# Kernel optimization log

Hardware: AMD Instinct MI355X
Metric: run time of the kernel (lower is better)

## Reference

```python
import jax, jax.numpy as jnp
import numpy as np

C, NHEAD, WIN = 192, 6, 8

def setup_inputs() -> dict:
    key = jax.random.key(0)
    ks = jax.random.split(key, 16)
    B, H, W = 4, 256, 256
    s = 0.02
    inp = {
        "q2d": jax.random.normal(ks[0], (B, C, H, W), jnp.float32),
        "kv2d": jax.random.normal(ks[1], (B, C, H, W), jnp.float32),
        "wq": jax.random.normal(ks[2], (C, C), jnp.float32) * s,
        "bq": jnp.zeros((C,), jnp.float32),
        "wk": jax.random.normal(ks[3], (C, C), jnp.float32) * s,
        "bk": jnp.zeros((C,), jnp.float32),
        "wv": jax.random.normal(ks[4], (C, C), jnp.float32) * s,
        "bv": jnp.zeros((C,), jnp.float32),
        "in_w": jax.random.normal(ks[5], (3 * C, C), jnp.float32) * s,
        "in_b": jnp.zeros((3 * C,), jnp.float32),
        "out_w": jax.random.normal(ks[6], (C, C), jnp.float32) * s,
        "out_b": jnp.zeros((C,), jnp.float32),
        "proj_w": jax.random.normal(ks[7], (C, C), jnp.float32) * s,
        "proj_b": jnp.zeros((C,), jnp.float32),
    }
    return inp

def _conv1x1(x, w, b):
    # x: [B,C,H,W], w: [O,C] (1x1 conv kernel), b: [O]
    return jnp.einsum('bchw,oc->bohw', x, w) + b[None, :, None, None]

def reference(q2d, kv2d, wq, bq, wk, bk, wv, bv, in_w, in_b, out_w, out_b, proj_w, proj_b):
    B, c, H, W = q2d.shape
    w = WIN
    Hb, Wb = H // w, W // w  # H,W chosen divisible by window -> pad is a no-op
    L = Hb * Wb
    S = w * w
    hd = c // NHEAD

    q = _conv1x1(q2d, wq, bq)
    k = _conv1x1(kv2d, wk, bk)
    v = _conv1x1(kv2d, wv, bv)

    def to_seq(t):
        # unfold(kernel=w, stride=w) -> blocks row-major over (Hb, Wb), tokens row-major within window
        return t.reshape(B, c, Hb, w, Wb, w).transpose(0, 2, 4, 3, 5, 1).reshape(B * L, S, c)

    qs, ks_, vs = to_seq(q), to_seq(k), to_seq(v)

    # nn.MultiheadAttention internal projections
    wq_i, wk_i, wv_i = jnp.split(in_w, 3, axis=0)
    bq_i, bk_i, bv_i = jnp.split(in_b, 3, axis=0)

    def heads(t, wgt, b):
        return (t @ wgt.T + b).reshape(B * L, S, NHEAD, hd).transpose(0, 2, 1, 3)

    qh = heads(qs, wq_i, bq_i)
    kh = heads(ks_, wk_i, bk_i)
    vh = heads(vs, wv_i, bv_i)

    scores = jnp.einsum('nhsd,nhtd->nhst', qh, kh) / jnp.sqrt(jnp.float32(hd))
    attn = jax.nn.softmax(scores, axis=-1)
    o = jnp.einsum('nhst,nhtd->nhsd', attn, vh)
    o = o.transpose(0, 2, 1, 3).reshape(B * L, S, c) @ out_w.T + out_b

    # fold back: [B*L, S, C] -> [B, C, H, W]
    o2d = o.reshape(B, Hb, Wb, w, w, c).transpose(0, 5, 1, 3, 2, 4).reshape(B, c, H, W)
    out = _conv1x1(o2d, proj_w, proj_b)
    return out + q2d
```

## Files before the change

kernel.cpp:

```cpp
#include <hip/hip_runtime.h>

#define CC 192
#define WFRAG_USHORTS (4*6*12*512)
#define SX 202
#define SV 74

typedef __attribute__((ext_vector_type(8))) short bf16x8;
typedef __attribute__((ext_vector_type(4))) float f32x4;

__device__ __forceinline__ unsigned short f2b(float f){
  unsigned u = __float_as_uint(f);
  return (unsigned short)((u + 0x7fffu + ((u >> 16) & 1u)) >> 16);
}
__device__ __forceinline__ unsigned pk2(float a, float b){
  return (unsigned)f2b(a) | ((unsigned)f2b(b) << 16);
}

__global__ void fuse_weights(const float* __restrict__ wq, const float* __restrict__ bq,
                             const float* __restrict__ wk, const float* __restrict__ bk,
                             const float* __restrict__ wv, const float* __restrict__ bv,
                             const float* __restrict__ in_w, const float* __restrict__ in_b,
                             const float* __restrict__ out_w, const float* __restrict__ out_b,
                             const float* __restrict__ proj_w, const float* __restrict__ proj_b,
                             unsigned short* __restrict__ Wf, float* __restrict__ Bf)
{
  int mat = blockIdx.x / CC, o = blockIdx.x % CC, ci = threadIdx.x;
  const float *A, *Bm, *bs, *ba; int aoff, boff; float scale = 1.f;
  if (mat == 0){ A=in_w; aoff=0;    Bm=wq;    bs=bq;    ba=in_b;   boff=0;    scale=0.17677669529663687f; }
  else if (mat==1){ A=in_w; aoff=CC;   Bm=wk;    bs=bk;    ba=in_b;   boff=CC;   }
  else if (mat==2){ A=in_w; aoff=2*CC; Bm=wv;    bs=bv;    ba=in_b;   boff=2*CC; }
  else            { A=proj_w; aoff=0;  Bm=out_w; bs=out_b; ba=proj_b; boff=0;    }
  const float* ar = A + (size_t)(aoff + o) * CC;
  float acc = 0.f;
  for (int m = 0; m < CC; ++m) acc = fmaf(ar[m], Bm[m*CC + ci], acc);
  int k = ci >> 5, n = o >> 4, lgv = (ci >> 3) & 3, e = ci & 7;
  int lane = (o & 15) | (lgv << 4);
  Wf[(((mat*6 + k)*12 + n) << 9) + lane*8 + e] = f2b(acc * scale);
  if (ci == 0){
    float bacc = 0.f;
    for (int m = 0; m < CC; ++m) bacc = fmaf(ar[m], bs[m], bacc);
    Bf[mat*CC + o] = (bacc + ba[boff + o]) * scale;
  }
}

__global__ __launch_bounds__(512, 4) void win_attn(
    const float* __restrict__ q2d, const float* __restrict__ kv2d,
    const unsigned short* __restrict__ Wf, const float* __restrict__ Bf,
    float* __restrict__ out)
{
  __shared__ unsigned short QK[2][64*SX];
  __shared__ unsigned short VT[192*SV];

  const int t = threadIdx.x;
  const int w = t >> 6, lane = t & 63, lr = lane & 15, lg = lane >> 4;
  const int bid = blockIdx.x;
  const int wid = (bid & 7) * 512 + (bid >> 3);
  const int b = wid >> 10, l = wid & 1023;
  const int y0 = (l >> 5) << 3, x0 = (l & 31) << 3;
  const float* qsrc  = q2d  + (size_t)b * CC * 65536;
  const float* kvsrc = kv2d + (size_t)b * CC * 65536;

  const int mat = w >> 2;
  const int tb  = 3 * (w & 3);

  auto stage = [&](const float* __restrict__ src, unsigned short* __restrict__ dst){
    #pragma unroll
    for (int i = 0; i < 3; ++i){
      int lin = i*512 + t;
      int c2 = lin >> 4, tok0 = (lin & 15) << 2;
      int gy = (y0 + (tok0 >> 3)) * 256 + x0 + (tok0 & 7);
      float4 va = *(const float4*)&src[(size_t)(2*c2)   * 65536 + gy];
      float4 vb = *(const float4*)&src[(size_t)(2*c2+1) * 65536 + gy];
      float fa[4] = {va.x, va.y, va.z, va.w};
      float fb[4] = {vb.x, vb.y, vb.z, vb.w};
      #pragma unroll
      for (int j = 0; j < 4; ++j)
        *(unsigned*)&dst[(tok0 + j)*SX + 2*c2] = pk2(fa[j], fb[j]);
    }
  };

  stage(qsrc,  QK[0]);
  stage(kvsrc, QK[1]);
  __syncthreads();

  const unsigned short* Xs = QK[mat];
  f32x4 qk[3][4] = {};
  f32x4 vv[3][2] = {};
  #pragma unroll
  for (int k = 0; k < 6; ++k){
    bf16x8 a[4];
    #pragma unroll
    for (int m = 0; m < 4; ++m)
      a[m] = *(const bf16x8*)&Xs[(m*16 + lr)*SX + k*32 + lg*8];
    bf16x8 av[2];
    #pragma unroll
    for (int mi = 0; mi < 2; ++mi)
      av[mi] = *(const bf16x8*)&QK[1][((2*mat + mi)*16 + lr)*SX + k*32 + lg*8];
    #pragma unroll
    for (int i = 0; i < 3; ++i){
      bf16x8 bw = *(const bf16x8*)&Wf[(((mat*6 + k)*12 + tb + i) << 9) + lane*8];
      #pragma unroll
      for (int m = 0; m < 4; ++m)
        qk[i][m] = __builtin_amdgcn_mfma_f32_16x16x32_bf16(a[m], bw, qk[i][m], 0, 0, 0);
      bf16x8 bv = *(const bf16x8*)&Wf[(((12 + k)*12 + tb + i) << 9) + lane*8];
      #pragma unroll
      for (int mi = 0; mi < 2; ++mi)
        vv[i][mi] = __builtin_amdgcn_mfma_f32_16x16x32_bf16(av[mi], bv, vv[i][mi], 0, 0, 0);
    }
  }
  #pragma unroll
  for (int i = 0; i < 3; ++i){
    int ch = (tb + i)*16 + lr;
    float bb = Bf[2*CC + ch];
    #pragma unroll
    for (int mi = 0; mi < 2; ++mi){
      int tk = (2*mat + mi)*16 + lg*4;
      *(unsigned*)&VT[ch*SV + tk]     = pk2(vv[i][mi][0] + bb, vv[i][mi][1] + bb);
      *(unsigned*)&VT[ch*SV + tk + 2] = pk2(vv[i][mi][2] + bb, vv[i][mi][3] + bb);
    }
  }
  __syncthreads();

  {
    unsigned short* dst = QK[mat];
    #pragma unroll
    for (int i = 0; i < 3; ++i){
      int ch = (tb + i)*16 + lr;
      float bb = Bf[mat*CC + ch];
      #pragma unroll
      for (int m = 0; m < 4; ++m)
        #pragma unroll
        for (int rr = 0; rr < 4; ++rr)
          dst[(m*16 + lg*4 + rr)*SX + ch] = f2b(qk[i][m][rr] + bb);
    }
  }
  __syncthreads();

  #pragma unroll
  for (int i = 0; i < 3; ++i){
    int task = 3*w + i;
    int h = task >> 2, r0 = (task & 3) << 4;
    f32x4 st[4] = {};
    bf16x8 bq_ = *(const bf16x8*)&QK[0][(r0 + lr)*SX + h*32 + lg*8];
    #pragma unroll
    for (int m = 0; m < 4; ++m){
      bf16x8 a = *(const bf16x8*)&QK[1][(m*16 + lr)*SX + h*32 + lg*8];
      st[m] = __builtin_amdgcn_mfma_f32_16x16x32_bf16(a, bq_, st[m], 0, 0, 0);
    }
    float mx = st[0][0];
    #pragma unroll
    for (int m = 0; m < 4; ++m)
      #pragma unroll
      for (int rr = 0; rr < 4; ++rr) mx = fmaxf(mx, st[m][rr]);
    mx = fmaxf(mx, __shfl_xor(mx, 16));
    mx = fmaxf(mx, __shfl_xor(mx, 32));
    float p[16]; float s = 0.f;
    #pragma unroll
    for (int m = 0; m < 4; ++m)
      #pragma unroll
      for (int rr = 0; rr < 4; ++rr){ float e = __expf(st[m][rr] - mx); p[m*4+rr] = e; s += e; }
    s += __shfl_xor(s, 16); s += __shfl_xor(s, 32);
    float inv = 1.f / s;
    #pragma unroll
    for (int i2 = 0; i2 < 16; ++i2) p[i2] *= inv;
    f32x4 o0 = {}, o1 = {};
    #pragma unroll
    for (int kt = 0; kt < 2; ++kt){
      bf16x8 ap;
      ((unsigned*)&ap)[0] = pk2(p[8*kt+0], p[8*kt+1]);
      ((unsigned*)&ap)[1] = pk2(p[8*kt+2], p[8*kt+3]);
      ((unsigned*)&ap)[2] = pk2(p[8*kt+4], p[8*kt+5]);
      ((unsigned*)&ap)[3] = pk2(p[8*kt+6], p[8*kt+7]);
      bf16x8 v0, v1;
      ((uint2*)&v0)[0] = *(const uint2*)&VT[(h*32 + lr)*SV      + kt*32 + lg*4];
      ((uint2*)&v0)[1] = *(const uint2*)&VT[(h*32 + lr)*SV      + kt*32 + 16 + lg*4];
      ((uint2*)&v1)[0] = *(const uint2*)&VT[(h*32 + 16 + lr)*SV + kt*32 + lg*4];
      ((uint2*)&v1)[1] = *(const uint2*)&VT[(h*32 + 16 + lr)*SV + kt*32 + 16 + lg*4];
      o0 = __builtin_amdgcn_mfma_f32_16x16x32_bf16(ap, v0, o0, 0, 0, 0);
      o1 = __builtin_amdgcn_mfma_f32_16x16x32_bf16(ap, v1, o1, 0, 0, 0);
    }
    #pragma unroll
    for (int rr = 0; rr < 4; ++rr){
      int tok = r0 + lg*4 + rr;
      QK[0][tok*SX + h*32 + lr]      = f2b(o0[rr]);
      QK[0][tok*SX + h*32 + 16 + lr] = f2b(o1[rr]);
    }
  }
  __syncthreads();

  {
    f32x4 eo[3][2] = {};
    #pragma unroll
    for (int k = 0; k < 6; ++k){
      bf16x8 bo[2];
      #pragma unroll
      for (int nt = 0; nt < 2; ++nt)
        bo[nt] = *(const bf16x8*)&QK[0][((2*mat + nt)*16 + lr)*SX + k*32 + lg*8];
      #pragma unroll
      for (int i = 0; i < 3; ++i){
        bf16x8 aw = *(const bf16x8*)&Wf[(((18 + k)*12 + tb + i) << 9) + lane*8];
        #pragma unroll
        for (int nt = 0; nt < 2; ++nt)
          eo[i][nt] = __builtin_amdgcn_mfma_f32_16x16x32_bf16(aw, bo[nt], eo[i][nt], 0, 0, 0);
      }
    }
    #pragma unroll
    for (int i = 0; i < 3; ++i){
      #pragma unroll
      for (int rr = 0; rr < 4; ++rr){
        int o = (tb + i)*16 + lg*4 + rr;
        float bb = Bf[3*CC + o];
        #pragma unroll
        for (int nt = 0; nt < 2; ++nt){
          int tok = (2*mat + nt)*16 + lr;
          size_t g = (size_t)(b*CC + o)*65536 + (size_t)(y0 + (tok >> 3))*256 + x0 + (tok & 7);
          out[g] = eo[i][nt][rr] + bb + q2d[g];
        }
      }
    }
  }
}

extern "C" void kernel_launch(void* const* d_in, const int* in_sizes, int n_in,
                              void* d_out, int out_size, void* d_ws, size_t ws_size,
                              hipStream_t stream)
{
  const float* q2d    = (const float*)d_in[0];
  const float* kv2d   = (const float*)d_in[1];
  const float* wq     = (const float*)d_in[2];
  const float* bq     = (const float*)d_in[3];
  const float* wk     = (const float*)d_in[4];
  const float* bk     = (const float*)d_in[5];
  const float* wv     = (const float*)d_in[6];
  const float* bv     = (const float*)d_in[7];
  const float* in_w   = (const float*)d_in[8];
  const float* in_b   = (const float*)d_in[9];
  const float* out_w  = (const float*)d_in[10];
  const float* out_b  = (const float*)d_in[11];
  const float* proj_w = (const float*)d_in[12];
  const float* proj_b = (const float*)d_in[13];

  unsigned short* Wf = (unsigned short*)d_ws;
  float* Bf = (float*)((char*)d_ws + WFRAG_USHORTS*2);
  float* out = (float*)d_out;

  fuse_weights<<<4*CC, CC, 0, stream>>>(wq,bq,wk,bk,wv,bv,in_w,in_b,
                                        out_w,out_b,proj_w,proj_b, Wf, Bf);
  win_attn<<<4096, 512, 0, stream>>>(q2d, kv2d, Wf, Bf, out);
}
```

Measured before the change: 347.0 us.

## Use six waves per window, keep V in registers, drop VT shared buffer

Shrinks the block from 8 to 6 waves so each wave owns one head's 32 channels, and computes V, Q and K projections in sequence over all 64 tokens. Each wave keeps its V tile in registers as MFMA B operands instead of writing a transposed VT array to LDS, and Q/K are written back in place with extra barriers. Removing VT cuts LDS per block, which is meant to let more blocks fit per CU (launch bounds 384,5). In exchange, register pressure per wave rises and each wave carries more serial MFMA work.

```diff
diff --git a/kernel.cpp b/kernel.cpp
--- a/kernel.cpp
+++ b/kernel.cpp
@@ -3,7 +3,6 @@
 #define CC 192
 #define WFRAG_USHORTS (4*6*12*512)
 #define SX 202
-#define SV 74
 
 typedef __attribute__((ext_vector_type(8))) short bf16x8;
 typedef __attribute__((ext_vector_type(4))) float f32x4;
@@ -43,13 +42,12 @@
   }
 }
 
-__global__ __launch_bounds__(512, 4) void win_attn(
+__global__ __launch_bounds__(384, 5) void win_attn(
     const float* __restrict__ q2d, const float* __restrict__ kv2d,
     const unsigned short* __restrict__ Wf, const float* __restrict__ Bf,
     float* __restrict__ out)
 {
   __shared__ unsigned short QK[2][64*SX];
-  __shared__ unsigned short VT[192*SV];
 
   const int t = threadIdx.x;
   const int w = t >> 6, lane = t & 63, lr = lane & 15, lg = lane >> 4;
@@ -59,14 +57,12 @@
   const int y0 = (l >> 5) << 3, x0 = (l & 31) << 3;
   const float* qsrc  = q2d  + (size_t)b * CC * 65536;
   const float* kvsrc = kv2d + (size_t)b * CC * 65536;
-
-  const int mat = w >> 2;
-  const int tb  = 3 * (w & 3);
+  const int tb2 = 2 * w;
 
   auto stage = [&](const float* __restrict__ src, unsigned short* __restrict__ dst){
     #pragma unroll
-    for (int i = 0; i < 3; ++i){
-      int lin = i*512 + t;
+    for (int i = 0; i < 4; ++i){
+      int lin = i*384 + t;
       int c2 = lin >> 4, tok0 = (lin & 15) << 2;
       int gy = (y0 + (tok0 >> 3)) * 256 + x0 + (tok0 & 7);
       float4 va = *(const float4*)&src[(size_t)(2*c2)   * 65536 + gy];
@@ -83,136 +79,169 @@
   stage(kvsrc, QK[1]);
   __syncthreads();
 
-  const unsigned short* Xs = QK[mat];
-  f32x4 qk[3][4] = {};
-  f32x4 vv[3][2] = {};
+  bf16x8 vp[2][2];
+  {
+    f32x4 vacc[2][4] = {};
+    #pragma unroll
+    for (int k = 0; k < 6; ++k){
+      bf16x8 a[4];
+      #pragma unroll
+      for (int m = 0; m < 4; ++m)
+        a[m] = *(const bf16x8*)&QK[1][(m*16 + lr)*SX + k*32 + lg*8];
+      #pragma unroll
+      for (int i = 0; i < 2; ++i){
+        bf16x8 bw = *(const bf16x8*)&Wf[(((12 + k)*12 + tb2 + i) << 9) + lane*8];
+        #pragma unroll
+        for (int m = 0; m < 4; ++m)
+          vacc[i][m] = __builtin_amdgcn_mfma_f32_16x16x32_bf16(a[m], bw, vacc[i][m], 0, 0, 0);
+      }
+    }
+    #pragma unroll
+    for (int i = 0; i < 2; ++i){
+      float bb = Bf[2*CC + (tb2 + i)*16 + lr];
+      #pragma unroll
+      for (int kt = 0; kt < 2; ++kt){
+        bf16x8 v;
+        ((unsigned*)&v)[0] = pk2(vacc[i][2*kt][0] + bb,   vacc[i][2*kt][1] + bb);
+        ((unsigned*)&v)[1] = pk2(vacc[i][2*kt][2] + bb,   vacc[i][2*kt][3] + bb);
+        ((unsigned*)&v)[2] = pk2(vacc[i][2*kt+1][0] + bb, vacc[i][2*kt+1][1] + bb);
+        ((unsigned*)&v)[3] = pk2(vacc[i][2*kt+1][2] + bb, vacc[i][2*kt+1][3] + bb);
+        vp[i][kt] = v;
+      }
+    }
+  }
+
+  f32x4 qacc[2][4] = {};
   #pragma unroll
   for (int k = 0; k < 6; ++k){
     bf16x8 a[4];
     #pragma unroll
     for (int m = 0; m < 4; ++m)
-      a[m] = *(const bf16x8*)&Xs[(m*16 + lr)*SX + k*32 + lg*8];
-    bf16x8 av[2];
-    #pragma unroll
-    for (int mi = 0; mi < 2; ++mi)
-      av[mi] = *(const bf16x8*)&QK[1][((2*mat + mi)*16 + lr)*SX + k*32 + lg*8];
-    #pragma unroll
-    for (int i = 0; i < 3; ++i){
-      bf16x8 bw = *(const bf16x8*)&Wf[(((mat*6 + k)*12 + tb + i) << 9) + lane*8];
-      #pragma unroll
-      for (int m = 0; m < 4; ++m)
-        qk[i][m] = __builtin_amdgcn_mfma_f32_16x16x32_bf16(a[m], bw, qk[i][m], 0, 0, 0);
-      bf16x8 bv = *(const bf16x8*)&Wf[(((12 + k)*12 + tb + i) << 9) + lane*8];
-      #pragma unroll
-      for (int mi = 0; mi < 2; ++mi)
-        vv[i][mi] = __builtin_amdgcn_mfma_f32_16x16x32_bf16(av[mi], bv, vv[i][mi], 0, 0, 0);
-    }
-  }
-  #pragma unroll
-  for (int i = 0; i < 3; ++i){
-    int ch = (tb + i)*16 + lr;
-    float bb = Bf[2*CC + ch];
-    #pragma unroll
-    for (int mi = 0; mi < 2; ++mi){
-      int tk = (2*mat + mi)*16 + lg*4;
-      *(unsigned*)&VT[ch*SV + tk]     = pk2(vv[i][mi][0] + bb, vv[i][mi][1] + bb);
-      *(unsigned*)&VT[ch*SV + tk + 2] = pk2(vv[i][mi][2] + bb, vv[i][mi][3] + bb);
-    }
+      a[m] = *(const bf16x8*)&QK[0][(m*16 + lr)*SX + k*32 + lg*8];
+    #pragma unroll
+    for (int i = 0; i < 2; ++i){
+      bf16x8 bw = *(const bf16x8*)&Wf[(((0*6 + k)*12 + tb2 + i) << 9) + lane*8];
+      #pragma unroll
+      for (int m = 0; m < 4; ++m)
+        qacc[i][m] = __builtin_amdgcn_mfma_f32_16x16x32_bf16(a[m], bw, qacc[i][m], 0, 0, 0);
+    }
+  }
+  __syncthreads();
+  #pragma unroll
+  for (int i = 0; i < 2; ++i){
+    int ch = (tb2 + i)*16 + lr;
+    float bb = Bf[0*CC + ch];
+    #pragma unroll
+    for (int m = 0; m < 4; ++m)
+      #pragma unroll
+      for (int rr = 0; rr < 4; ++rr)
+        QK[0][(m*16 + lg*4 + rr)*SX + ch] = f2b(qacc[i][m][rr] + bb);
+  }
+
+  f32x4 kacc[2][4] = {};
+  #pragma unroll
+  for (int k = 0; k < 6; ++k){
+    bf16x8 a[4];
+    #pragma unroll
+    for (int m = 0; m < 4; ++m)
+      a[m] = *(const bf16x8*)&QK[1][(m*16 + lr)*SX + k*32 + lg*8];
+    #pragma unroll
+    for (int i = 0; i < 2; ++i){
+      bf16x8 bw = *(const bf16x8*)&Wf[(((1*6 + k)*12 + tb2 + i) << 9) + lane*8];
+      #pragma unroll
+      for (int m = 0; m < 4; ++m)
+        kacc[i][m] = __builtin_amdgcn_mfma_f32_16x16x32_bf16(a[m], bw, kacc[i][m], 0, 0, 0);
+    }
+  }
+  __syncthreads();
+  #pragma unroll
+  for (int i = 0; i < 2; ++i){
+    int ch = (tb2 + i)*16 + lr;
+    float bb = Bf[1*CC + ch];
+    #pragma unroll
+    for (int m = 0; m < 4; ++m)
+      #pragma unroll
+      for (int rr = 0; rr < 4; ++rr)
+        QK[1][(m*16 + lg*4 + rr)*SX + ch] = f2b(kacc[i][m][rr] + bb);
   }
   __syncthreads();
 
   {
-    unsigned short* dst = QK[mat];
-    #pragma unroll
-    for (int i = 0; i < 3; ++i){
-      int ch = (tb + i)*16 + lr;
-      float bb = Bf[mat*CC + ch];
-      #pragma unroll
-      for (int m = 0; m < 4; ++m)
-        #pragma unroll
-        for (int rr = 0; rr < 4; ++rr)
-          dst[(m*16 + lg*4 + rr)*SX + ch] = f2b(qk[i][m][rr] + bb);
-    }
-  }
-  __syncthreads();
-
-  #pragma unroll
-  for (int i = 0; i < 3; ++i){
-    int task = 3*w + i;
-    int h = task >> 2, r0 = (task & 3) << 4;
-    f32x4 st[4] = {};
-    bf16x8 bq_ = *(const bf16x8*)&QK[0][(r0 + lr)*SX + h*32 + lg*8];
-    #pragma unroll
-    for (int m = 0; m < 4; ++m){
-      bf16x8 a = *(const bf16x8*)&QK[1][(m*16 + lr)*SX + h*32 + lg*8];
-      st[m] = __builtin_amdgcn_mfma_f32_16x16x32_bf16(a, bq_, st[m], 0, 0, 0);
-    }
-    float mx = st[0][0];
-    #pragma unroll
-    for (int m = 0; m < 4; ++m)
-      #pragma unroll
-      for (int rr = 0; rr < 4; ++rr) mx = fmaxf(mx, st[m][rr]);
-    mx = fmaxf(mx, __shfl_xor(mx, 16));
-    mx = fmaxf(mx, __shfl_xor(mx, 32));
-    float p[16]; float s = 0.f;
-    #pragma unroll
-    for (int m = 0; m < 4; ++m)
-      #pragma unroll
-      for (int rr = 0; rr < 4; ++rr){ float e = __expf(st[m][rr] - mx); p[m*4+rr] = e; s += e; }
-    s += __shfl_xor(s, 16); s += __shfl_xor(s, 32);
-    float inv = 1.f / s;
-    #pragma unroll
-    for (int i2 = 0; i2 < 16; ++i2) p[i2] *= inv;
-    f32x4 o0 = {}, o1 = {};
-    #pragma unroll
-    for (int kt = 0; kt < 2; ++kt){
-      bf16x8 ap;
-      ((unsigned*)&ap)[0] = pk2(p[8*kt+0], p[8*kt+1]);
-      ((unsigned*)&ap)[1] = pk2(p[8*kt+2], p[8*kt+3]);
-      ((unsigned*)&ap)[2] = pk2(p[8*kt+4], p[8*kt+5]);
-      ((unsigned*)&ap)[3] = pk2(p[8*kt+6], p[8*kt+7]);
-      bf16x8 v0, v1;
-      ((uint2*)&v0)[0] = *(const uint2*)&VT[(h*32 + lr)*SV      + kt*32 + lg*4];
-      ((uint2*)&v0)[1] = *(const uint2*)&VT[(h*32 + lr)*SV      + kt*32 + 16 + lg*4];
-      ((uint2*)&v1)[0] = *(const uint2*)&VT[(h*32 + 16 + lr)*SV + kt*32 + lg*4];
-      ((uint2*)&v1)[1] = *(const uint2*)&VT[(h*32 + 16 + lr)*SV + kt*32 + 16 + lg*4];
-      o0 = __builtin_amdgcn_mfma_f32_16x16x32_bf16(ap, v0, o0, 0, 0, 0);
-      o1 = __builtin_amdgcn_mfma_f32_16x16x32_bf16(ap, v1, o1, 0, 0, 0);
-    }
-    #pragma unroll
-    for (int rr = 0; rr < 4; ++rr){
-      int tok = r0 + lg*4 + rr;
-      QK[0][tok*SX + h*32 + lr]      = f2b(o0[rr]);
-      QK[0][tok*SX + h*32 + 16 + lr] = f2b(o1[rr]);
+    const int h = w;
+    bf16x8 ka[4];
+    #pragma unroll
+    for (int m = 0; m < 4; ++m)
+      ka[m] = *(const bf16x8*)&QK[1][(m*16 + lr)*SX + h*32 + lg*8];
+    #pragma unroll
+    for (int r = 0; r < 4; ++r){
+      const int r0 = r << 4;
+      f32x4 st[4] = {};
+      bf16x8 bq_ = *(const bf16x8*)&QK[0][(r0 + lr)*SX + h*32 + lg*8];
+      #pragma unroll
+      for (int m = 0; m < 4; ++m)
+        st[m] = __builtin_amdgcn_mfma_f32_16x16x32_bf16(ka[m], bq_, st[m], 0, 0, 0);
+      float mx = st[0][0];
+      #pragma unroll
+      for (int m = 0; m < 4; ++m)
+        #pragma unroll
+        for (int rr = 0; rr < 4; ++rr) mx = fmaxf(mx, st[m][rr]);
+      mx = fmaxf(mx, __shfl_xor(mx, 16));
+      mx = fmaxf(mx, __shfl_xor(mx, 32));
+      float p[16]; float s = 0.f;
+      #pragma unroll
+      for (int m = 0; m < 4; ++m)
+        #pragma unroll
+        for (int rr = 0; rr < 4; ++rr){ float e = __expf(st[m][rr] - mx); p[m*4+rr] = e; s += e; }
+      s += __shfl_xor(s, 16); s += __shfl_xor(s, 32);
+      float inv = 1.f / s;
+      #pragma unroll
+      for (int i2 = 0; i2 < 16; ++i2) p[i2] *= inv;
+      f32x4 o0 = {}, o1 = {};
+      #pragma unroll
+      for (int kt = 0; kt < 2; ++kt){
+        bf16x8 ap;
+        ((unsigned*)&ap)[0] = pk2(p[8*kt+0], p[8*kt+1]);
+        ((unsigned*)&ap)[1] = pk2(p[8*kt+2], p[8*kt+3]);
+        ((unsigned*)&ap)[2] = pk2(p[8*kt+4], p[8*kt+5]);
+        ((unsigned*)&ap)[3] = pk2(p[8*kt+6], p[8*kt+7]);
+        o0 = __builtin_amdgcn_mfma_f32_16x16x32_bf16(ap, vp[0][kt], o0, 0, 0, 0);
+        o1 = __builtin_amdgcn_mfma_f32_16x16x32_bf16(ap, vp[1][kt], o1, 0, 0, 0);
+      }
+      #pragma unroll
+      for (int rr = 0; rr < 4; ++rr){
+        int tok = r0 + lg*4 + rr;
+        QK[0][tok*SX + h*32 + lr]      = f2b(o0[rr]);
+        QK[0][tok*SX + h*32 + 16 + lr] = f2b(o1[rr]);
+      }
     }
   }
   __syncthreads();
 
   {
-    f32x4 eo[3][2] = {};
+    f32x4 eo[2][4] = {};
     #pragma unroll
     for (int k = 0; k < 6; ++k){
-      bf16x8 bo[2];
-      #pragma unroll
-      for (int nt = 0; nt < 2; ++nt)
-        bo[nt] = *(const bf16x8*)&QK[0][((2*mat + nt)*16 + lr)*SX + k*32 + lg*8];
-      #pragma unroll
-      for (int i = 0; i < 3; ++i){
-        bf16x8 aw = *(const bf16x8*)&Wf[(((18 + k)*12 + tb + i) << 9) + lane*8];
-        #pragma unroll
-        for (int nt = 0; nt < 2; ++nt)
+      bf16x8 bo[4];
+      #pragma unroll
+      for (int nt = 0; nt < 4; ++nt)
+        bo[nt] = *(const bf16x8*)&QK[0][(nt*16 + lr)*SX + k*32 + lg*8];
+      #pragma unroll
+      for (int i = 0; i < 2; ++i){
+        bf16x8 aw = *(const bf16x8*)&Wf[(((18 + k)*12 + tb2 + i) << 9) + lane*8];
+        #pragma unroll
+        for (int nt = 0; nt < 4; ++nt)
           eo[i][nt] = __builtin_amdgcn_mfma_f32_16x16x32_bf16(aw, bo[nt], eo[i][nt], 0, 0, 0);
       }
     }
     #pragma unroll
-    for (int i = 0; i < 3; ++i){
+    for (int i = 0; i < 2; ++i){
       #pragma unroll
       for (int rr = 0; rr < 4; ++rr){
-        int o = (tb + i)*16 + lg*4 + rr;
+        int o = (tb2 + i)*16 + lg*4 + rr;
         float bb = Bf[3*CC + o];
         #pragma unroll
-        for (int nt = 0; nt < 2; ++nt){
-          int tok = (2*mat + nt)*16 + lr;
+        for (int nt = 0; nt < 4; ++nt){
+          int tok = nt*16 + lr;
           size_t g = (size_t)(b*CC + o)*65536 + (size_t)(y0 + (tok >> 3))*256 + x0 + (tok & 7);
           out[g] = eo[i][nt][rr] + bb + q2d[g];
         }
@@ -246,5 +275,5 @@
 
   fuse_weights<<<4*CC, CC, 0, stream>>>(wq,bq,wk,bk,wv,bv,in_w,in_b,
                                         out_w,out_b,proj_w,proj_b, Wf, Bf);
-  win_attn<<<4096, 512, 0, stream>>>(q2d, kv2d, Wf, Bf, out);
-}
+  win_attn<<<4096, 384, 0, stream>>>(q2d, kv2d, Wf, Bf, out);
+}
```

Measured after the change: 467.9 us. 1.35x slower.
